# Optimization experiments

Hardware: AMD Instinct MI355X
Metric: run time of the kernel (lower is better)

## Reference

```python
import jax, jax.numpy as jnp
import numpy as np

B, C, H, W = 4, 64, 256, 256
HEADS, DHEAD = 4, 64
INNER = HEADS * DHEAD


def setup_inputs() -> dict:
    key = jax.random.key(0)
    ks = jax.random.split(key, 8)
    s = 1.0 / np.sqrt(C)
    return {
        "x_in": jax.random.normal(ks[0], (B, C, H, W), jnp.float32),
        "illu_fea_trans": jax.random.normal(ks[1], (B, C, H, W), jnp.float32),
        "Wq": jax.random.normal(ks[2], (C, INNER), jnp.float32) * s,
        "Wk": jax.random.normal(ks[3], (C, INNER), jnp.float32) * s,
        "Wv": jax.random.normal(ks[4], (C, INNER), jnp.float32) * s,
        "WL": jax.random.normal(ks[5], (C, INNER), jnp.float32) * s,
        "rescale": jnp.ones((HEADS, 1, 1), jnp.float32),
        "Wp": jax.random.normal(ks[6], (INNER, C), jnp.float32) / np.sqrt(INNER),
        "bp": jnp.zeros((C,), jnp.float32),
    }


def _l2norm(t, axis=-1, eps=1e-12):
    # matches torch F.normalize(p=2): x / max(||x||, eps)
    n = jnp.sqrt(jnp.sum(t * t, axis=axis, keepdims=True))
    return t / jnp.maximum(n, eps)


def reference(x_in, illu_fea_trans, Wq, Wk, Wv, WL, rescale, Wp, bp):
    b, c, h, w = x_in.shape
    n = h * w
    # NCHW -> [b, n, c]
    x = jnp.transpose(x_in, (0, 2, 3, 1)).reshape(b, n, c)
    illu = jnp.transpose(illu_fea_trans, (0, 2, 3, 1)).reshape(b, n, c)

    def split_heads(t):  # [b,n,inner] -> [b,heads,d,n] (transposed attention)
        return jnp.transpose(t.reshape(b, n, HEADS, DHEAD), (0, 2, 3, 1))

    q = split_heads(x @ Wq)           # [b,h,d,n]
    k = split_heads(x @ Wk)
    v = split_heads(x @ Wv) * split_heads(illu @ WL)  # illumination-gated v

    q = _l2norm(q, axis=-1)
    k = _l2norm(k, axis=-1)
    attn = jnp.einsum('bhdn,bhen->bhde', k, q)  # [b,h,d,d]
    attn = jax.nn.softmax(attn * rescale[None], axis=-1)
    out = jnp.einsum('bhde,bhen->bhdn', attn, v)  # [b,h,d,n]

    # [b,h,d,n] -> [b,n,inner]
    out = jnp.transpose(out, (0, 3, 1, 2)).reshape(b, n, INNER)
    out = out @ Wp + bp  # [b,n,c]
    return jnp.transpose(out.reshape(b, h, w, c), (0, 3, 1, 2))  # [b,c,h,w]
```

## Files before the change

### kernel.cpp

```cpp
#include <hip/hip_runtime.h>
#include <hip/hip_bf16.h>


#define NPOS 65536
#define CH 64
#define INNER 256

typedef __attribute__((ext_vector_type(8))) __bf16 bfrag;
typedef __attribute__((ext_vector_type(4))) float facc;
typedef __attribute__((ext_vector_type(4))) float fvec4;

typedef const __attribute__((address_space(1))) unsigned int guint;
typedef __attribute__((address_space(3))) unsigned int luint;

__device__ __forceinline__ unsigned short f2bu(float f) {
  return __builtin_bit_cast(unsigned short, (__bf16)f);
}

#define SWA(row, colbyte) ((row) * 128 + ((colbyte) ^ (((row) & 7) << 4)))

#define BAR_VM4()  asm volatile("s_waitcnt vmcnt(4)\n\ts_barrier" ::: "memory")
#define BAR_VM0()  asm volatile("s_waitcnt vmcnt(0)\n\ts_barrier" ::: "memory")
#define BAR_LGKM() asm volatile("s_waitcnt lgkmcnt(0)\n\ts_barrier" ::: "memory")

__global__ __launch_bounds__(256) void k0_wt(const float* __restrict__ Wv,
                                             const float* __restrict__ WL,
                                             unsigned short* __restrict__ WvT,
                                             unsigned short* __restrict__ WLT) {
  int t = blockIdx.x * 256 + threadIdx.x;
  int c = t >> 8, i = t & 255;
  WvT[i * CH + c] = f2bu(Wv[c * INNER + i]);
  WLT[i * CH + c] = f2bu(WL[c * INNER + i]);
}

__global__ __launch_bounds__(256) void k1_xx(const float* __restrict__ x,
                                             float* __restrict__ xx) {
  const int b = blockIdx.y;
  const int wave = threadIdx.x >> 6, lane = threadIdx.x & 63;
  const int r = lane & 15, g = lane >> 4;
  const int gw = blockIdx.x * 4 + wave;
  const int per = NPOS / 128;
  const size_t n0 = (size_t)gw * per;
  const float* xb = x + (size_t)b * CH * NPOS;

  facc acc[4][4] = {};

  for (int n = 0; n < per; n += 32) {
    bfrag fr[4];
#pragma unroll
    for (int t = 0; t < 4; ++t) {
      const float* p = xb + (size_t)(16 * t + r) * NPOS + n0 + n + g * 8;
      fvec4 lo = *(const fvec4*)p;
      fvec4 hi = *(const fvec4*)(p + 4);
      bfrag f;
#pragma unroll
      for (int e = 0; e < 4; ++e) { f[e] = (__bf16)lo[e]; f[e + 4] = (__bf16)hi[e]; }
      fr[t] = f;
    }
#pragma unroll
    for (int ti = 0; ti < 4; ++ti)
#pragma unroll
      for (int tj = 0; tj < 4; ++tj)
        acc[ti][tj] = __builtin_amdgcn_mfma_f32_16x16x32_bf16(fr[ti], fr[tj],
                                                              acc[ti][tj], 0, 0, 0);
  }

  __shared__ float red[4][4096];
  float* my = red[wave];
#pragma unroll
  for (int ti = 0; ti < 4; ++ti)
#pragma unroll
    for (int tj = 0; tj < 4; ++tj)
#pragma unroll
      for (int q = 0; q < 4; ++q)
        my[(16 * ti + g * 4 + q) * 64 + 16 * tj + r] = acc[ti][tj][q];
  __syncthreads();
  float* xxb = xx + (size_t)b * 4096;
  for (int i = threadIdx.x; i < 4096; i += 256)
    atomicAdd(xxb + i, red[0][i] + red[1][i] + red[2][i] + red[3][i]);
}

__global__ __launch_bounds__(256) void k2_attn(
    const float* __restrict__ xx, const float* __restrict__ Wq,
    const float* __restrict__ Wk, const float* __restrict__ rescale,
    const float* __restrict__ Wp, unsigned short* __restrict__ Mt) {
  const int b = blockIdx.x >> 2, h = blockIdx.x & 3;
  const int t = threadIdx.x;
  const int wave = t >> 6, lane = t & 63;
  const int r = lane & 15, g = lane >> 4;

  __shared__ __align__(16) char tXX[8192];
  __shared__ __align__(16) char tWq[8192];
  __shared__ __align__(16) char tWk[8192];
  __shared__ __align__(16) char tWp[8192];
  __shared__ __align__(16) char tZq[8192];
  __shared__ __align__(16) char tZk[8192];
  __shared__ __align__(16) char tAt[8192];
  __shared__ float gG[64][68];
  __shared__ float sMx[64][4], sSm[64][4];
  __shared__ float sNq[64], sNk[64];

  const float* xxb = xx + (size_t)b * 4096;
#pragma unroll
  for (int rep = 0; rep < 16; ++rep) {
    int idx = rep * 256 + t;
    int row = idx >> 6, col = idx & 63;
    *(unsigned short*)(tXX + SWA(row, col * 2)) = f2bu(xxb[idx]);
    float vq = Wq[row * INNER + h * 64 + col];
    float vk = Wk[row * INNER + h * 64 + col];
    *(unsigned short*)(tWq + SWA(col, row * 2)) = f2bu(vq);
    *(unsigned short*)(tWk + SWA(col, row * 2)) = f2bu(vk);
    *(unsigned short*)(tWp + SWA(col, row * 2)) = f2bu(Wp[(h * 64 + row) * CH + col]);
  }
  __syncthreads();

  facc zq[4] = {}, zk[4] = {};
#pragma unroll
  for (int s = 0; s < 2; ++s) {
    bfrag aq = *(const bfrag*)(tWq + SWA(16 * wave + r, s * 64 + g * 16));
    bfrag ak = *(const bfrag*)(tWk + SWA(16 * wave + r, s * 64 + g * 16));
#pragma unroll
    for (int tj = 0; tj < 4; ++tj) {
      bfrag bx = *(const bfrag*)(tXX + SWA(16 * tj + r, s * 64 + g * 16));
      zq[tj] = __builtin_amdgcn_mfma_f32_16x16x32_bf16(aq, bx, zq[tj], 0, 0, 0);
      zk[tj] = __builtin_amdgcn_mfma_f32_16x16x32_bf16(ak, bx, zk[tj], 0, 0, 0);
    }
  }
#pragma unroll
  for (int tj = 0; tj < 4; ++tj)
#pragma unroll
    for (int q = 0; q < 4; ++q) {
      int row = 16 * wave + g * 4 + q, colb = (16 * tj + r) * 2;
      *(unsigned short*)(tZq + SWA(row, colb)) = f2bu(zq[tj][q]);
      *(unsigned short*)(tZk + SWA(row, colb)) = f2bu(zk[tj][q]);
    }
  __syncthreads();

  facc ga[4] = {}, q2[4] = {}, k2[4] = {};
#pragma unroll
  for (int s = 0; s < 2; ++s) {
    bfrag azk = *(const bfrag*)(tZk + SWA(16 * wave + r, s * 64 + g * 16));
    bfrag azq = *(const bfrag*)(tZq + SWA(16 * wave + r, s * 64 + g * 16));
#pragma unroll
    for (int tj = 0; tj < 4; ++tj) {
      bfrag bq = *(const bfrag*)(tWq + SWA(16 * tj + r, s * 64 + g * 16));
      bfrag bk = *(const bfrag*)(tWk + SWA(16 * tj + r, s * 64 + g * 16));
      ga[tj] = __builtin_amdgcn_mfma_f32_16x16x32_bf16(azk, bq, ga[tj], 0, 0, 0);
      q2[tj] = __builtin_amdgcn_mfma_f32_16x16x32_bf16(azq, bq, q2[tj], 0, 0, 0);
      k2[tj] = __builtin_amdgcn_mfma_f32_16x16x32_bf16(azk, bk, k2[tj], 0, 0, 0);
    }
  }
#pragma unroll
  for (int tj = 0; tj < 4; ++tj)
#pragma unroll
    for (int q = 0; q < 4; ++q) {
      int row = 16 * wave + g * 4 + q, col = 16 * tj + r;
      gG[row][col] = ga[tj][q];
      if (row == col) { sNq[row] = q2[tj][q]; sNk[row] = k2[tj][q]; }
    }
  __syncthreads();

  if (t < 64) {
    sNq[t] = 1.f / fmaxf(sqrtf(sNq[t]), 1e-12f);
    sNk[t] = rescale[h] / fmaxf(sqrtf(sNk[t]), 1e-12f);
  }
  __syncthreads();

  {
    const int d = t >> 2, p = t & 3;
    const float ik = sNk[d];
    float le[16];
    float mx = -1e30f;
#pragma unroll
    for (int j = 0; j < 16; ++j) {
      float v = gG[d][16 * p + j] * ik * sNq[16 * p + j];
      le[j] = v; mx = fmaxf(mx, v);
    }
    sMx[d][p] = mx;
    __syncthreads();
    mx = fmaxf(fmaxf(sMx[d][0], sMx[d][1]), fmaxf(sMx[d][2], sMx[d][3]));
    float sm = 0.f;
#pragma unroll
    for (int j = 0; j < 16; ++j) { le[j] = __expf(le[j] - mx); sm += le[j]; }
    sSm[d][p] = sm;
    __syncthreads();
    sm = sSm[d][0] + sSm[d][1] + sSm[d][2] + sSm[d][3];
    const float inv = 1.f / sm;
#pragma unroll
    for (int j = 0; j < 16; ++j) {
      int e = 16 * p + j;
      *(unsigned short*)(tAt + SWA(e, d * 2)) = f2bu(le[j] * inv);
    }
  }
  __syncthreads();

  facc m[4] = {};
#pragma unroll
  for (int s = 0; s < 2; ++s) {
    bfrag aa = *(const bfrag*)(tAt + SWA(16 * wave + r, s * 64 + g * 16));
#pragma unroll
    for (int tj = 0; tj < 4; ++tj) {
      bfrag bw = *(const bfrag*)(tWp + SWA(16 * tj + r, s * 64 + g * 16));
      m[tj] = __builtin_amdgcn_mfma_f32_16x16x32_bf16(aa, bw, m[tj], 0, 0, 0);
    }
  }
#pragma unroll
  for (int tj = 0; tj < 4; ++tj)
#pragma unroll
    for (int q = 0; q < 4; ++q) {
      int e = 16 * wave + g * 4 + q, c2 = 16 * tj + r;
      Mt[((size_t)(b * CH + c2)) * INNER + h * 64 + e] = f2bu(m[tj][q]);
    }
}

__global__ __launch_bounds__(256) void k3_out(
    const float* __restrict__ x, const float* __restrict__ illu,
    const unsigned short* __restrict__ WvT, const unsigned short* __restrict__ WLT,
    const unsigned short* __restrict__ Mt, const float* __restrict__ bp,
    float* __restrict__ out) {
  const int b = blockIdx.y;
  const int wave = threadIdx.x >> 6, lane = threadIdx.x & 63;
  const int r = lane & 15, g = lane >> 4;
  const int n0 = blockIdx.x * 256;

  __shared__ __align__(16) float xf[2][64][32];
  __shared__ __align__(16) float ifl[2][64][32];
  __shared__ __align__(16) char lvs[2][8192];

  bfrag wvA[4][2], wlA[4][2], mtA[8];
#pragma unroll
  for (int ti = 0; ti < 4; ++ti) {
    const int i = wave * 64 + ti * 16 + r;
#pragma unroll
    for (int s = 0; s < 2; ++s) {
      wvA[ti][s] = *(const bfrag*)(WvT + i * CH + s * 32 + g * 8);
      wlA[ti][s] = *(const bfrag*)(WLT + i * CH + s * 32 + g * 8);
    }
  }
#pragma unroll
  for (int s8 = 0; s8 < 8; ++s8)
    mtA[s8] = *(const bfrag*)(Mt + ((size_t)(b * CH + wave * 16 + r)) * INNER + s8 * 32 + g * 8);
  float bcol[4];
#pragma unroll
  for (int q = 0; q < 4; ++q) bcol[q] = bp[wave * 16 + g * 4 + q];

  const float* xb = x + (size_t)b * CH * NPOS;
  const float* ib = illu + (size_t)b * CH * NPOS;
  float* ob = out + (size_t)b * CH * NPOS;

  const int c0 = wave * 16 + (lane >> 3);
  const int c1 = c0 + 8;
  const int k0_ = (c0 >> 3) & 3, k1_ = (c1 >> 3) & 3;
  const int fk0 = k0_ ^ ((k0_ & 1) << 2), fk1 = k1_ ^ ((k1_ & 1) << 2);
  const size_t off0 = (size_t)c0 * NPOS + (((lane & 7) ^ fk0) << 2);
  const size_t off1 = (size_t)c1 * NPOS + (((lane & 7) ^ fk1) << 2);

#define ISSUE(BUF, NC)                                                        \
  {                                                                           \
    __builtin_amdgcn_global_load_lds((guint*)(xb + off0 + (NC)),              \
        (luint*)&xf[BUF][wave * 16][0], 16, 0, 0);                            \
    __builtin_amdgcn_global_load_lds((guint*)(xb + off1 + (NC)),              \
        (luint*)&xf[BUF][wave * 16 + 8][0], 16, 0, 0);                        \
    __builtin_amdgcn_global_load_lds((guint*)(ib + off0 + (NC)),              \
        (luint*)&ifl[BUF][wave * 16][0], 16, 0, 0);                           \
    __builtin_amdgcn_global_load_lds((guint*)(ib + off1 + (NC)),              \
        (luint*)&ifl[BUF][wave * 16 + 8][0], 16, 0, 0);                       \
  }

  ISSUE(0, n0);
  BAR_VM0();

  const int fkr = g ^ ((g & 1) << 2);

  for (int cc = 0; cc < 8; ++cc) {
    const int cb = cc & 1;
    const int nbase = n0 + cc * 32;
    if (cc < 7) ISSUE(cb ^ 1, nbase + 32);
    BAR_VM4();

#pragma unroll 2
    for (int sub = 0; sub < 2; ++sub) {
      const int j0 = sub * 16;
      const int j = j0 + r;
      const int qw = ((((j >> 2) ^ fkr) << 2) | (j & 3));
      bfrag xB[2], iB[2];
#pragma unroll
      for (int s = 0; s < 2; ++s) {
        float xw[8], iw[8];
#pragma unroll
        for (int e = 0; e < 8; ++e) {
          const int c = s * 32 + g * 8 + e;
          xw[e] = xf[cb][c][qw];
          iw[e] = ifl[cb][c][qw];
        }
        bfrag fx, fi;
#pragma unroll
        for (int e = 0; e < 8; ++e) { fx[e] = (__bf16)xw[e]; fi[e] = (__bf16)iw[e]; }
        xB[s] = fx; iB[s] = fi;
      }
      facc av[4] = {}, gv[4] = {};
      __builtin_amdgcn_s_setprio(1);
#pragma unroll
      for (int ti = 0; ti < 4; ++ti) {
#pragma unroll
        for (int s = 0; s < 2; ++s) {
          av[ti] = __builtin_amdgcn_mfma_f32_16x16x32_bf16(wvA[ti][s], xB[s], av[ti], 0, 0, 0);
          gv[ti] = __builtin_amdgcn_mfma_f32_16x16x32_bf16(wlA[ti][s], iB[s], gv[ti], 0, 0, 0);
        }
      }
      __builtin_amdgcn_s_setprio(0);
#pragma unroll
      for (int ti = 0; ti < 4; ++ti) {
        const float v0 = av[ti][0] * gv[ti][0], v1 = av[ti][1] * gv[ti][1];
        const float v2 = av[ti][2] * gv[ti][2], v3 = av[ti][3] * gv[ti][3];
        const int i = wave * 64 + ti * 16 + g * 4;
        const int sw = (r & 7) << 4;
        unsigned long long pk =
            (unsigned long long)((unsigned int)f2bu(v0) | ((unsigned int)f2bu(v1) << 16)) |
            ((unsigned long long)((unsigned int)f2bu(v2) | ((unsigned int)f2bu(v3) << 16)) << 32);
        *(unsigned long long*)(lvs[sub] + r * 512 + ((i * 2) ^ sw)) = pk;
      }
      BAR_LGKM();
      facc ov = {0.f, 0.f, 0.f, 0.f};
      __builtin_amdgcn_s_setprio(1);
#pragma unroll
      for (int s8 = 0; s8 < 8; ++s8) {
        const int byte = (s8 * 64 + g * 16) ^ ((r & 7) << 4);
        bfrag vB = *(const bfrag*)(lvs[sub] + r * 512 + byte);
        ov = __builtin_amdgcn_mfma_f32_16x16x32_bf16(mtA[s8], vB, ov, 0, 0, 0);
      }
      __builtin_amdgcn_s_setprio(0);
#pragma unroll
      for (int q = 0; q < 4; ++q)
        ob[(size_t)(wave * 16 + g * 4 + q) * NPOS + nbase + j0 + r] = ov[q] + bcol[q];
    }
  }
#undef ISSUE
}

extern "C" void kernel_launch(void* const* d_in, const int* in_sizes, int n_in,
                              void* d_out, int out_size, void* d_ws, size_t ws_size,
                              hipStream_t stream) {
  (void)in_sizes; (void)n_in; (void)out_size; (void)ws_size;
  const float* x    = (const float*)d_in[0];
  const float* illu = (const float*)d_in[1];
  const float* Wq   = (const float*)d_in[2];
  const float* Wk   = (const float*)d_in[3];
  const float* Wv   = (const float*)d_in[4];
  const float* WL   = (const float*)d_in[5];
  const float* rsc  = (const float*)d_in[6];
  const float* Wp   = (const float*)d_in[7];
  const float* bp   = (const float*)d_in[8];
  float* out = (float*)d_out;

  float* xxws = (float*)d_ws;
  unsigned short* Mt  = (unsigned short*)((char*)d_ws + 65536);
  unsigned short* WvT = (unsigned short*)((char*)d_ws + 65536 + 131072);
  unsigned short* WLT = WvT + INNER * CH;

  hipMemsetAsync(d_ws, 0, (size_t)4 * 4096 * sizeof(float), stream);
  hipLaunchKernelGGL(k0_wt, dim3(64), dim3(256), 0, stream, Wv, WL, WvT, WLT);
  hipLaunchKernelGGL(k1_xx, dim3(32, 4), dim3(256), 0, stream, x, xxws);
  hipLaunchKernelGGL(k2_attn, dim3(16), dim3(256), 0, stream, xxws, Wq, Wk, rsc, Wp, Mt);
  hipLaunchKernelGGL(k3_out, dim3(256, 4), dim3(256), 0, stream, x, illu, WvT, WLT, Mt, bp, out);
}
```

Before: 85.48 us.

## Fuse output projection into register MFMA chain with cross-wave LDS reduction

The gated value tile is no longer staged through LDS as bf16 for a second MFMA pass. Each wave now multiplies its own 64-row slice of gated v directly by the matching slice of Mt with 16x16x16 MFMAs. It then reduces the partial outputs across the four waves through a small fp32 LDS buffer and writes float4 outputs. This removes the bf16 LDS round trip and changes the store pattern to vectorised rows. In exchange it adds a second barrier per sub-tile and fp32 reduction traffic in LDS.

```diff
diff --git a/kernel.cpp b/kernel.cpp
--- a/kernel.cpp
+++ b/kernel.cpp
@@ -9,6 +9,7 @@
 typedef __attribute__((ext_vector_type(8))) __bf16 bfrag;
 typedef __attribute__((ext_vector_type(4))) float facc;
 typedef __attribute__((ext_vector_type(4))) float fvec4;
+typedef __attribute__((ext_vector_type(4))) short sh4;
 
 typedef const __attribute__((address_space(1))) unsigned int guint;
 typedef __attribute__((address_space(3))) unsigned int luint;
@@ -16,6 +17,17 @@
 __device__ __forceinline__ unsigned short f2bu(float f) {
   return __builtin_bit_cast(unsigned short, (__bf16)f);
 }
+
+#if __has_builtin(__builtin_amdgcn_mfma_f32_16x16x16bf16_1k)
+__device__ __forceinline__ facc mfma16(sh4 a, sh4 b, facc c) {
+  return __builtin_amdgcn_mfma_f32_16x16x16bf16_1k(a, b, c, 0, 0, 0);
+}
+#else
+__device__ __forceinline__ facc mfma16(sh4 a, sh4 b, facc c) {
+  asm("v_mfma_f32_16x16x16_bf16 %0, %1, %2, %0" : "+v"(c) : "v"(a), "v"(b));
+  return c;
+}
+#endif
 
 #define SWA(row, colbyte) ((row) * 128 + ((colbyte) ^ (((row) & 7) << 4)))
 
@@ -225,9 +237,10 @@
 
   __shared__ __align__(16) float xf[2][64][32];
   __shared__ __align__(16) float ifl[2][64][32];
-  __shared__ __align__(16) char lvs[2][8192];
-
-  bfrag wvA[4][2], wlA[4][2], mtA[8];
+  __shared__ __align__(16) fvec4 red[4][4][64];
+
+  bfrag wvA[4][2], wlA[4][2];
+  sh4 mtB[4][4];
 #pragma unroll
   for (int ti = 0; ti < 4; ++ti) {
     const int i = wave * 64 + ti * 16 + r;
@@ -236,13 +249,12 @@
       wvA[ti][s] = *(const bfrag*)(WvT + i * CH + s * 32 + g * 8);
       wlA[ti][s] = *(const bfrag*)(WLT + i * CH + s * 32 + g * 8);
     }
-  }
-#pragma unroll
-  for (int s8 = 0; s8 < 8; ++s8)
-    mtA[s8] = *(const bfrag*)(Mt + ((size_t)(b * CH + wave * 16 + r)) * INNER + s8 * 32 + g * 8);
-  float bcol[4];
-#pragma unroll
-  for (int q = 0; q < 4; ++q) bcol[q] = bp[wave * 16 + g * 4 + q];
+#pragma unroll
+    for (int ct = 0; ct < 4; ++ct)
+      mtB[ti][ct] = *(const sh4*)(Mt + ((size_t)(b * CH + ct * 16 + r)) * INNER +
+                                  wave * 64 + ti * 16 + g * 4);
+  }
+  const float bias = bp[wave * 16 + r];
 
   const float* xb = x + (size_t)b * CH * NPOS;
   const float* ib = illu + (size_t)b * CH * NPOS;
@@ -298,41 +310,42 @@
         for (int e = 0; e < 8; ++e) { fx[e] = (__bf16)xw[e]; fi[e] = (__bf16)iw[e]; }
         xB[s] = fx; iB[s] = fi;
       }
-      facc av[4] = {}, gv[4] = {};
+      facc pout[4] = {};
       __builtin_amdgcn_s_setprio(1);
 #pragma unroll
       for (int ti = 0; ti < 4; ++ti) {
+        facc av = {}, gv = {};
 #pragma unroll
         for (int s = 0; s < 2; ++s) {
-          av[ti] = __builtin_amdgcn_mfma_f32_16x16x32_bf16(wvA[ti][s], xB[s], av[ti], 0, 0, 0);
-          gv[ti] = __builtin_amdgcn_mfma_f32_16x16x32_bf16(wlA[ti][s], iB[s], gv[ti], 0, 0, 0);
+          av = __builtin_amdgcn_mfma_f32_16x16x32_bf16(wvA[ti][s], xB[s], av, 0, 0, 0);
+          gv = __builtin_amdgcn_mfma_f32_16x16x32_bf16(wlA[ti][s], iB[s], gv, 0, 0, 0);
         }
+        sh4 a2;
+#pragma unroll
+        for (int e = 0; e < 4; ++e) a2[e] = (short)f2bu(av[e] * gv[e]);
+#pragma unroll
+        for (int ct = 0; ct < 4; ++ct)
+          pout[ct] = mfma16(a2, mtB[ti][ct], pout[ct]);
       }
       __builtin_amdgcn_s_setprio(0);
 #pragma unroll
-      for (int ti = 0; ti < 4; ++ti) {
-        const float v0 = av[ti][0] * gv[ti][0], v1 = av[ti][1] * gv[ti][1];
-        const float v2 = av[ti][2] * gv[ti][2], v3 = av[ti][3] * gv[ti][3];
-        const int i = wave * 64 + ti * 16 + g * 4;
-        const int sw = (r & 7) << 4;
-        unsigned long long pk =
-            (unsigned long long)((unsigned int)f2bu(v0) | ((unsigned int)f2bu(v1) << 16)) |
-            ((unsigned long long)((unsigned int)f2bu(v2) | ((unsigned int)f2bu(v3) << 16)) << 32);
-        *(unsigned long long*)(lvs[sub] + r * 512 + ((i * 2) ^ sw)) = pk;
+      for (int d = 1; d < 4; ++d) {
+        const int ct = (wave + d) & 3;
+        red[ct][wave][lane] = pout[ct];
       }
       BAR_LGKM();
-      facc ov = {0.f, 0.f, 0.f, 0.f};
-      __builtin_amdgcn_s_setprio(1);
-#pragma unroll
-      for (int s8 = 0; s8 < 8; ++s8) {
-        const int byte = (s8 * 64 + g * 16) ^ ((r & 7) << 4);
-        bfrag vB = *(const bfrag*)(lvs[sub] + r * 512 + byte);
-        ov = __builtin_amdgcn_mfma_f32_16x16x32_bf16(mtA[s8], vB, ov, 0, 0, 0);
+      fvec4 tot = pout[wave];
+#pragma unroll
+      for (int d = 1; d < 4; ++d) {
+        const int w2 = (wave + d) & 3;
+        fvec4 p = red[wave][w2][lane];
+        tot += p;
       }
-      __builtin_amdgcn_s_setprio(0);
-#pragma unroll
-      for (int q = 0; q < 4; ++q)
-        ob[(size_t)(wave * 16 + g * 4 + q) * NPOS + nbase + j0 + r] = ov[q] + bcol[q];
+      fvec4 o;
+#pragma unroll
+      for (int q = 0; q < 4; ++q) o[q] = tot[q] + bias;
+      *(fvec4*)(ob + (size_t)(wave * 16 + r) * NPOS + nbase + j0 + g * 4) = o;
+      BAR_LGKM();
     }
   }
 #undef ISSUE
```

Result: slower. 173.1 us (+102.5%).
